# Kernel optimization log

Hardware: AMD Instinct MI355X
Metric: run time of the kernel (lower is better)

The kernel has to match this reference:

```python
import math
import jax, jax.numpy as jnp
import numpy as np

N_FREQS = 16
MAX_PERIOD = 4096.0
INJECTION_SCALE = 1.0


def setup_inputs() -> dict:
    key = jax.random.key(0)
    ks = jax.random.split(key, 5)
    B, L, D, K = 4, 8192, 1024, 2
    read_in = K * 2 * N_FREQS  # 64
    x = jax.random.normal(ks[0], (B, L, D), dtype=jnp.float32)
    # Linear weights stored as (in, out) so y = x @ W + b (== torch x @ W.T + b)
    inc_w = jax.random.normal(ks[1], (D, K), dtype=jnp.float32) * 0.02
    inc_b = jnp.full((K,), -2.0, dtype=jnp.float32)   # nn.init.constant_(inc_proj.bias, -2.0)
    reset_w = jax.random.normal(ks[2], (D, K), dtype=jnp.float32) * 0.02
    reset_b = jnp.full((K,), -5.0, dtype=jnp.float32)  # nn.init.constant_(reset_proj.bias, -5.0)
    read_w = jax.random.normal(ks[3], (read_in, D), dtype=jnp.float32) * 0.02
    read_b = jnp.zeros((D,), dtype=jnp.float32)
    return {"x": x, "inc_w": inc_w, "inc_b": inc_b, "reset_w": reset_w,
            "reset_b": reset_b, "read_w": read_w, "read_b": read_b}


def reference(x, inc_w, inc_b, reset_w, reset_b, read_w, read_b):
    # Gates from hidden state
    inc_logits = x @ inc_w + inc_b        # (B, L, K)
    reset_logits = x @ reset_w + reset_b  # (B, L, K)
    inc = jax.nn.sigmoid(inc_logits)
    keep = 1.0 - jax.nn.sigmoid(reset_logits)

    # Diagonal linear recurrence c[t] = keep[t]*c[t-1] + inc[t]
    # expressed as an associative scan over affine maps f(x) = k*x + i.
    def combine(left, right):
        kl, il = left
        kr, ir = right
        return (kl * kr, ir + kr * il)

    _, counters = jax.lax.associative_scan(combine, (keep, inc), axis=1)  # (B, L, K)

    # Sinusoidal readout: (B, L, K) -> (B, L, K*2*n_freqs)
    freqs = jnp.exp(jnp.linspace(0.0, math.log(MAX_PERIOD), N_FREQS)).astype(x.dtype)
    sc = counters[..., None] / freqs                       # (B, L, K, F)
    emb = jnp.concatenate([jnp.sin(sc), jnp.cos(sc)], -1)  # (B, L, K, 2F)
    B, L, K, _ = emb.shape
    emb = emb.reshape(B, L, K * 2 * N_FREQS)

    injection = INJECTION_SCALE * (emb @ read_w + read_b)  # (B, L, d_model)
    return injection, inc_logits, counters
```

## Files before the change

### kernel.cpp

```cpp
#include <hip/hip_runtime.h>

#define B_    4
#define L_    8192
#define D_    1024
#define ROWS_ 32768
#define NCH_  128

typedef __attribute__((ext_vector_type(8))) short  short8;
typedef __attribute__((ext_vector_type(4))) float  floatx4;

__device__ __forceinline__ unsigned short f2bf(float f){
  unsigned int u = __float_as_uint(f);
  u += 0x7fffu + ((u >> 16) & 1u);
  return (unsigned short)(u >> 16);
}

__global__ __launch_bounds__(512) void k_gates(
    const float* __restrict__ x,
    const float* __restrict__ inc_w, const float* __restrict__ inc_b,
    const float* __restrict__ reset_w, const float* __restrict__ reset_b,
    float* __restrict__ out_incl,
    float* __restrict__ cl, float* __restrict__ kc,
    float* __restrict__ sumP, float* __restrict__ sumQ,
    const float* __restrict__ read_w, unsigned short* __restrict__ Bt)
{
  const int blk  = blockIdx.x;
  if (blk >= 512){
    const int idx0 = ((blk - 512)*512 + threadIdx.x)*4;
    const int n  = idx0 >> 6;
    const int kk = idx0 & 63;
    ushort4 v;
    v.x = f2bf(read_w[(size_t)(kk+0)*D_ + n]);
    v.y = f2bf(read_w[(size_t)(kk+1)*D_ + n]);
    v.z = f2bf(read_w[(size_t)(kk+2)*D_ + n]);
    v.w = f2bf(read_w[(size_t)(kk+3)*D_ + n]);
    *(ushort4*)(Bt + idx0) = v;
    return;
  }

  __shared__ float s_keep[128];
  __shared__ float s_inc[128];
  const int b    = blk >> 7;
  const int ch   = blk & 127;
  const int tid  = threadIdx.x;
  const int w    = tid >> 6;
  const int lane = tid & 63;

  float4 wia[4], wib[4], wra[4], wrb[4];
  #pragma unroll
  for (int i = 0; i < 4; ++i){
    const int d0 = i*256 + lane*4;
    const float4* pi = (const float4*)(inc_w + d0*2);
    wia[i] = pi[0]; wib[i] = pi[1];
    const float4* pr = (const float4*)(reset_w + d0*2);
    wra[i] = pr[0]; wrb[i] = pr[1];
  }
  const float bi0 = inc_b[0], bi1 = inc_b[1];
  const float br0 = reset_b[0], br1 = reset_b[1];

  const int row0 = b*L_ + ch*64 + w*8;
  float4 xc[4], xn[4];
  {
    const float4* xr = (const float4*)(x + (size_t)row0 * D_);
    #pragma unroll
    for (int i = 0; i < 4; ++i) xc[i] = xr[i*64 + lane];
  }
  #pragma unroll
  for (int r = 0; r < 8; ++r){
    if (r < 7){
      const float4* xr = (const float4*)(x + (size_t)(row0 + r + 1) * D_);
      #pragma unroll
      for (int i = 0; i < 4; ++i) xn[i] = xr[i*64 + lane];
    }
    float ai0=0.f, ai1=0.f, ar0=0.f, ar1=0.f;
    #pragma unroll
    for (int i = 0; i < 4; ++i){
      const float4 v = xc[i];
      ai0 += v.x*wia[i].x + v.y*wia[i].z + v.z*wib[i].x + v.w*wib[i].z;
      ai1 += v.x*wia[i].y + v.y*wia[i].w + v.z*wib[i].y + v.w*wib[i].w;
      ar0 += v.x*wra[i].x + v.y*wra[i].z + v.z*wrb[i].x + v.w*wrb[i].z;
      ar1 += v.x*wra[i].y + v.y*wra[i].w + v.z*wrb[i].y + v.w*wrb[i].w;
    }
    #pragma unroll
    for (int m = 1; m < 64; m <<= 1){
      ai0 += __shfl_xor(ai0, m);
      ai1 += __shfl_xor(ai1, m);
      ar0 += __shfl_xor(ar0, m);
      ar1 += __shfl_xor(ar1, m);
    }
    if (lane == 0){
      const int row = row0 + r;
      const float il0 = ai0 + bi0, il1 = ai1 + bi1;
      const float rl0 = ar0 + br0, rl1 = ar1 + br1;
      out_incl[(size_t)row*2 + 0] = il0;
      out_incl[(size_t)row*2 + 1] = il1;
      const int lr = w*8 + r;
      s_inc [lr*2+0] = 1.f / (1.f + __expf(-il0));
      s_inc [lr*2+1] = 1.f / (1.f + __expf(-il1));
      s_keep[lr*2+0] = 1.f - 1.f / (1.f + __expf(-rl0));
      s_keep[lr*2+1] = 1.f - 1.f / (1.f + __expf(-rl1));
    }
    #pragma unroll
    for (int i = 0; i < 4; ++i) xc[i] = xn[i];
  }
  __syncthreads();

  if (tid < 128){
    const int k = w;
    float P = s_keep[lane*2 + k];
    float Q = s_inc [lane*2 + k];
    #pragma unroll
    for (int ofs = 1; ofs < 64; ofs <<= 1){
      const float Pp = __shfl_up(P, ofs);
      const float Qp = __shfl_up(Q, ofs);
      if (lane >= ofs){ Q = Q + P * Qp; P = P * Pp; }
    }
    const int row = b*L_ + ch*64 + lane;
    cl[(size_t)row*2 + k] = Q;
    kc[(size_t)row*2 + k] = P;
    if (lane == 63){
      const int seq = b*2 + k;
      sumP[seq*NCH_ + ch] = P;
      sumQ[seq*NCH_ + ch] = Q;
    }
  }
}

__global__ __launch_bounds__(256) void k_fused(
    const float* __restrict__ cl, const float* __restrict__ kc,
    const float* __restrict__ sumP, const float* __restrict__ sumQ,
    const unsigned short* __restrict__ Bt,
    const float* __restrict__ read_b,
    float* __restrict__ out_cnt, float* __restrict__ out)
{
  __shared__ float s_carry[2];
  const int tid  = threadIdx.x;
  const int w    = tid >> 6;
  const int lane = tid & 63;
  const int rowBase = blockIdx.x * 16;
  const int b   = rowBase >> 13;
  const int ch  = (rowBase & (L_ - 1)) >> 6;
  const int m    = lane & 15;
  const int quad = lane >> 4;

  if (w < 2){
    const int seq = b*2 + w;
    const float* P0 = sumP + seq*NCH_;
    const float* Q0 = sumQ + seq*NCH_;
    float P = P0[lane], Q = Q0[lane];
    #pragma unroll
    for (int ofs = 1; ofs < 64; ofs <<= 1){
      const float Pp = __shfl_up(P, ofs);
      const float Qp = __shfl_up(Q, ofs);
      if (lane >= ofs){ Q = Q + P * Qp; P = P * Pp; }
    }
    float carry = 0.f;
    if (ch > 0 && ch <= 64) carry = __shfl(Q, ch-1);
    const float Qc = __shfl(Q, 63);
    float P2 = P0[64 + lane], Q2 = Q0[64 + lane];
    #pragma unroll
    for (int ofs = 1; ofs < 64; ofs <<= 1){
      const float Pp = __shfl_up(P2, ofs);
      const float Qp = __shfl_up(Q2, ofs);
      if (lane >= ofs){ Q2 = Q2 + P2 * Qp; P2 = P2 * Pp; }
    }
    Q2 = Q2 + P2 * Qc;
    if (ch >= 65) carry = __shfl(Q2, ch-65);
    if (lane == 0) s_carry[w] = carry;
  }
  __syncthreads();
  const float carry0 = s_carry[0];
  const float carry1 = s_carry[1];

  const int row = rowBase + m;
  const float2 clv = *(const float2*)(cl + (size_t)row*2);
  const float2 kcv = *(const float2*)(kc + (size_t)row*2);
  const float c0 = clv.x + kcv.x * carry0;
  const float c1 = clv.y + kcv.y * carry1;
  if (w == 0 && lane < 16){
    ((float2*)out_cnt)[row] = make_float2(c0, c1);
  }

  const float TWO_PI_INV = 0.15915494309189535f;
  const float STEP = 0.5743491774985175f;
  float invf = (quad & 1) ? 0.011841535573494211f  : 1.0f;
  const bool use_cos = (quad >> 1) != 0;
  short8 a0, a1;
  #pragma unroll
  for (int j = 0; j < 8; ++j){
    float r0 = c0 * invf * TWO_PI_INV; r0 -= floorf(r0);
    float r1 = c1 * invf * TWO_PI_INV; r1 -= floorf(r1);
    const float e0 = use_cos ? __builtin_amdgcn_cosf(r0) : __builtin_amdgcn_sinf(r0);
    const float e1 = use_cos ? __builtin_amdgcn_cosf(r1) : __builtin_amdgcn_sinf(r1);
    a0[j] = (short)f2bf(e0);
    a1[j] = (short)f2bf(e1);
    invf *= STEP;
  }

  const int colBase = w * 256;
  floatx4 acc[16];
  #pragma unroll
  for (int ct = 0; ct < 16; ++ct) acc[ct] = (floatx4){0.f,0.f,0.f,0.f};
  #pragma unroll
  for (int ct = 0; ct < 16; ++ct){
    const int n = colBase + ct*16 + m;
    const short8* bp = (const short8*)(Bt + (size_t)n * 64);
    const short8 b0 = bp[quad];
    const short8 b1 = bp[4 + quad];
    acc[ct] = __builtin_amdgcn_mfma_f32_16x16x32_bf16(a0, b0, acc[ct], 0, 0, 0);
    acc[ct] = __builtin_amdgcn_mfma_f32_16x16x32_bf16(a1, b1, acc[ct], 0, 0, 0);
  }

  #pragma unroll
  for (int ct = 0; ct < 16; ++ct){
    const int col  = colBase + ct*16 + m;
    const float bias = read_b[col];
    #pragma unroll
    for (int r = 0; r < 4; ++r){
      const int orow = rowBase + quad*4 + r;
      out[(size_t)orow*D_ + col] = acc[ct][r] + bias;
    }
  }
}

extern "C" void kernel_launch(void* const* d_in, const int* in_sizes, int n_in,
                              void* d_out, int out_size, void* d_ws, size_t ws_size,
                              hipStream_t stream) {
  const float* x       = (const float*)d_in[0];
  const float* inc_w   = (const float*)d_in[1];
  const float* inc_b   = (const float*)d_in[2];
  const float* reset_w = (const float*)d_in[3];
  const float* reset_b = (const float*)d_in[4];
  const float* read_w  = (const float*)d_in[5];
  const float* read_b  = (const float*)d_in[6];

  float* out      = (float*)d_out;
  float* out_incl = out + (size_t)ROWS_ * D_;
  float* out_cnt  = out_incl + ROWS_ * 2;

  char* ws = (char*)d_ws;
  float* cl    = (float*)(ws + 0);
  float* kc    = (float*)(ws + 262144);
  float* sumP  = (float*)(ws + 524288);
  float* sumQ  = (float*)(ws + 528384);
  unsigned short* Bt  = (unsigned short*)(ws + 532480);

  k_gates<<<dim3(544),  dim3(512), 0, stream>>>(x, inc_w, inc_b, reset_w, reset_b,
                                                out_incl, cl, kc, sumP, sumQ,
                                                read_w, Bt);
  k_fused<<<dim3(2048), dim3(256), 0, stream>>>(cl, kc, sumP, sumQ, Bt, read_b,
                                                out_cnt, out);
}
```

Baseline: 264.2 us.

## Reuse register-resident B tiles across row tiles and use nontemporal loads/stores

The fused kernel now has each block cover a 64-row stripe and half of the columns. The bf16 weight fragments and bias are loaded into registers once and reused across four 16-row tiles, so each block's carry scan is amortized over more rows and the grid is halved. The x reads in the gate kernel and the big output stores switch to nontemporal loads and stores to reduce cache pollution. The trade-off is higher register pressure from holding the B fragments, and fewer blocks available for latency hiding.

```diff
diff --git a/kernel.cpp b/kernel.cpp
--- a/kernel.cpp
+++ b/kernel.cpp
@@ -59,27 +59,27 @@
   const float br0 = reset_b[0], br1 = reset_b[1];
 
   const int row0 = b*L_ + ch*64 + w*8;
-  float4 xc[4], xn[4];
+  floatx4 xc[4], xn[4];
   {
-    const float4* xr = (const float4*)(x + (size_t)row0 * D_);
-    #pragma unroll
-    for (int i = 0; i < 4; ++i) xc[i] = xr[i*64 + lane];
+    const floatx4* xr = (const floatx4*)(x + (size_t)row0 * D_);
+    #pragma unroll
+    for (int i = 0; i < 4; ++i) xc[i] = __builtin_nontemporal_load(xr + i*64 + lane);
   }
   #pragma unroll
   for (int r = 0; r < 8; ++r){
     if (r < 7){
-      const float4* xr = (const float4*)(x + (size_t)(row0 + r + 1) * D_);
+      const floatx4* xr = (const floatx4*)(x + (size_t)(row0 + r + 1) * D_);
       #pragma unroll
-      for (int i = 0; i < 4; ++i) xn[i] = xr[i*64 + lane];
+      for (int i = 0; i < 4; ++i) xn[i] = __builtin_nontemporal_load(xr + i*64 + lane);
     }
     float ai0=0.f, ai1=0.f, ar0=0.f, ar1=0.f;
     #pragma unroll
     for (int i = 0; i < 4; ++i){
-      const float4 v = xc[i];
-      ai0 += v.x*wia[i].x + v.y*wia[i].z + v.z*wib[i].x + v.w*wib[i].z;
-      ai1 += v.x*wia[i].y + v.y*wia[i].w + v.z*wib[i].y + v.w*wib[i].w;
-      ar0 += v.x*wra[i].x + v.y*wra[i].z + v.z*wrb[i].x + v.w*wrb[i].z;
-      ar1 += v.x*wra[i].y + v.y*wra[i].w + v.z*wrb[i].y + v.w*wrb[i].w;
+      const floatx4 v = xc[i];
+      ai0 += v[0]*wia[i].x + v[1]*wia[i].z + v[2]*wib[i].x + v[3]*wib[i].z;
+      ai1 += v[0]*wia[i].y + v[1]*wia[i].w + v[2]*wib[i].y + v[3]*wib[i].w;
+      ar0 += v[0]*wra[i].x + v[1]*wra[i].z + v[2]*wrb[i].x + v[3]*wrb[i].z;
+      ar1 += v[0]*wra[i].y + v[1]*wra[i].w + v[2]*wrb[i].y + v[3]*wrb[i].w;
     }
     #pragma unroll
     for (int m = 1; m < 64; m <<= 1){
@@ -137,11 +137,14 @@
   const int tid  = threadIdx.x;
   const int w    = tid >> 6;
   const int lane = tid & 63;
-  const int rowBase = blockIdx.x * 16;
-  const int b   = rowBase >> 13;
-  const int ch  = (rowBase & (L_ - 1)) >> 6;
+  const int stripe = blockIdx.x >> 1;
+  const int half   = blockIdx.x & 1;
+  const int rowBase0 = stripe * 64;
+  const int b  = rowBase0 >> 13;
+  const int ch = stripe & 127;
   const int m    = lane & 15;
   const int quad = lane >> 4;
+  const int colBase = half*512 + w*128;
 
   if (w < 2){
     const int seq = b*2 + w;
@@ -172,53 +175,65 @@
   const float carry0 = s_carry[0];
   const float carry1 = s_carry[1];
 
-  const int row = rowBase + m;
-  const float2 clv = *(const float2*)(cl + (size_t)row*2);
-  const float2 kcv = *(const float2*)(kc + (size_t)row*2);
-  const float c0 = clv.x + kcv.x * carry0;
-  const float c1 = clv.y + kcv.y * carry1;
-  if (w == 0 && lane < 16){
-    ((float2*)out_cnt)[row] = make_float2(c0, c1);
+  short8 b0[8], b1[8];
+  float  bias[8];
+  #pragma unroll
+  for (int ct = 0; ct < 8; ++ct){
+    const int n = colBase + ct*16 + m;
+    const short8* bp = (const short8*)(Bt + (size_t)n * 64);
+    b0[ct]  = bp[quad];
+    b1[ct]  = bp[4 + quad];
+    bias[ct] = read_b[n];
   }
 
   const float TWO_PI_INV = 0.15915494309189535f;
   const float STEP = 0.5743491774985175f;
-  float invf = (quad & 1) ? 0.011841535573494211f  : 1.0f;
+  const float INVF0 = (quad & 1) ? 0.011841535573494211f  : 1.0f;
   const bool use_cos = (quad >> 1) != 0;
-  short8 a0, a1;
-  #pragma unroll
-  for (int j = 0; j < 8; ++j){
-    float r0 = c0 * invf * TWO_PI_INV; r0 -= floorf(r0);
-    float r1 = c1 * invf * TWO_PI_INV; r1 -= floorf(r1);
-    const float e0 = use_cos ? __builtin_amdgcn_cosf(r0) : __builtin_amdgcn_sinf(r0);
-    const float e1 = use_cos ? __builtin_amdgcn_cosf(r1) : __builtin_amdgcn_sinf(r1);
-    a0[j] = (short)f2bf(e0);
-    a1[j] = (short)f2bf(e1);
-    invf *= STEP;
-  }
-
-  const int colBase = w * 256;
-  floatx4 acc[16];
-  #pragma unroll
-  for (int ct = 0; ct < 16; ++ct) acc[ct] = (floatx4){0.f,0.f,0.f,0.f};
-  #pragma unroll
-  for (int ct = 0; ct < 16; ++ct){
-    const int n = colBase + ct*16 + m;
-    const short8* bp = (const short8*)(Bt + (size_t)n * 64);
-    const short8 b0 = bp[quad];
-    const short8 b1 = bp[4 + quad];
-    acc[ct] = __builtin_amdgcn_mfma_f32_16x16x32_bf16(a0, b0, acc[ct], 0, 0, 0);
-    acc[ct] = __builtin_amdgcn_mfma_f32_16x16x32_bf16(a1, b1, acc[ct], 0, 0, 0);
-  }
-
-  #pragma unroll
-  for (int ct = 0; ct < 16; ++ct){
-    const int col  = colBase + ct*16 + m;
-    const float bias = read_b[col];
-    #pragma unroll
-    for (int r = 0; r < 4; ++r){
-      const int orow = rowBase + quad*4 + r;
-      out[(size_t)orow*D_ + col] = acc[ct][r] + bias;
+
+  #pragma unroll
+  for (int rt = 0; rt < 4; ++rt){
+    const int rowBase = rowBase0 + rt*16;
+    const int row = rowBase + m;
+
+    const float2 clv = *(const float2*)(cl + (size_t)row*2);
+    const float2 kcv = *(const float2*)(kc + (size_t)row*2);
+    const float c0 = clv.x + kcv.x * carry0;
+    const float c1 = clv.y + kcv.y * carry1;
+    if (half == 0 && w == 0 && lane < 16){
+      ((float2*)out_cnt)[row] = make_float2(c0, c1);
+    }
+
+    float invf = INVF0;
+    short8 a0, a1;
+    #pragma unroll
+    for (int j = 0; j < 8; ++j){
+      float r0 = c0 * invf * TWO_PI_INV; r0 -= floorf(r0);
+      float r1 = c1 * invf * TWO_PI_INV; r1 -= floorf(r1);
+      const float e0 = use_cos ? __builtin_amdgcn_cosf(r0) : __builtin_amdgcn_sinf(r0);
+      const float e1 = use_cos ? __builtin_amdgcn_cosf(r1) : __builtin_amdgcn_sinf(r1);
+      a0[j] = (short)f2bf(e0);
+      a1[j] = (short)f2bf(e1);
+      invf *= STEP;
+    }
+
+    floatx4 acc[8];
+    #pragma unroll
+    for (int ct = 0; ct < 8; ++ct) acc[ct] = (floatx4){0.f,0.f,0.f,0.f};
+    #pragma unroll
+    for (int ct = 0; ct < 8; ++ct){
+      acc[ct] = __builtin_amdgcn_mfma_f32_16x16x32_bf16(a0, b0[ct], acc[ct], 0, 0, 0);
+      acc[ct] = __builtin_amdgcn_mfma_f32_16x16x32_bf16(a1, b1[ct], acc[ct], 0, 0, 0);
+    }
+
+    #pragma unroll
+    for (int ct = 0; ct < 8; ++ct){
+      const int col = colBase + ct*16 + m;
+      #pragma unroll
+      for (int r = 0; r < 4; ++r){
+        const int orow = rowBase + quad*4 + r;
+        __builtin_nontemporal_store(acc[ct][r] + bias[ct], &out[(size_t)orow*D_ + col]);
+      }
     }
   }
 }
@@ -248,6 +263,6 @@
   k_gates<<<dim3(544),  dim3(512), 0, stream>>>(x, inc_w, inc_b, reset_w, reset_b,
                                                 out_incl, cl, kc, sumP, sumQ,
                                                 read_w, Bt);
-  k_fused<<<dim3(2048), dim3(256), 0, stream>>>(cl, kc, sumP, sumQ, Bt, read_b,
+  k_fused<<<dim3(1024), dim3(256), 0, stream>>>(cl, kc, sumP, sumQ, Bt, read_b,
                                                 out_cnt, out);
 }
```

After: 253.3 us. -4.1%, faster.
